# Performance work log

Measured on AMD Instinct MI355X. Metric: run time of the kernel, lower is better.

The kernel has to match this reference:

```python
import jax, jax.numpy as jnp
import numpy as np

B, N, C = 16, 1024, 256

def setup_inputs() -> dict:
    key = jax.random.key(0)
    kq, kk, kv, km, kd = jax.random.split(key, 5)
    query = jax.random.normal(kq, (B, N, C), dtype=jnp.float32)
    key_t = jax.random.normal(kk, (B, N, C), dtype=jnp.float32)
    value = jax.random.normal(kv, (B, N, C), dtype=jnp.float32)
    mask = jax.random.randint(km, (B, N, N), 0, 2).astype(jnp.bool_)
    dis = jax.random.normal(kd, (B, N, N), dtype=jnp.float32)
    return {"query": query, "key": key_t, "value": value, "mask": mask, "dis": dis}

def reference(query, key, value, mask, dis):
    # scores = Q K^T + dis, then scale, mask, softmax, @ V
    scores = jnp.einsum('bqc,bkc->bqk', query, key)
    scores = (scores + dis) / jnp.sqrt(jnp.asarray(query.shape[-1], query.dtype))
    scores = jnp.where(mask, -jnp.inf, scores)
    p_attn = jax.nn.softmax(scores, axis=-1)
    p_val = jnp.einsum('bqk,bkc->bqc', p_attn, value)
    return (p_val, p_attn)
```

## Files before the change

### kernel.cpp

```cpp
#include <hip/hip_runtime.h>
#include <stdint.h>

#define B_ 16
#define N_ 1024
#define C_ 256

typedef __attribute__((ext_vector_type(8))) short short8;
typedef __attribute__((ext_vector_type(4))) float f32x4;

__device__ __forceinline__ short f2bf(float f) {
  uint32_t u = __builtin_bit_cast(uint32_t, f);
  u += 0x7fffu + ((u >> 16) & 1u);
  return (short)(u >> 16);
}

__global__ __launch_bounds__(256) void cast_kernel(const float* __restrict__ in,
                                                   short* __restrict__ out, int n8) {
  int i = blockIdx.x * 256 + threadIdx.x;
  if (i >= n8) return;
  const float4* p = (const float4*)(in + (size_t)i * 8);
  float4 a = p[0], b = p[1];
  short8 r;
  r[0] = f2bf(a.x); r[1] = f2bf(a.y); r[2] = f2bf(a.z); r[3] = f2bf(a.w);
  r[4] = f2bf(b.x); r[5] = f2bf(b.y); r[6] = f2bf(b.z); r[7] = f2bf(b.w);
  *(short8*)(out + (size_t)i * 8) = r;
}

__global__ __launch_bounds__(256) void vt_kernel(const float* __restrict__ V,
                                                 short* __restrict__ Vt) {
  __shared__ float tile[32][33];
  int b = blockIdx.z;
  int nb = blockIdx.x * 32;
  int cb = blockIdx.y * 32;
  int tx = threadIdx.x & 31;
  int ty = threadIdx.x >> 5;
#pragma unroll
  for (int i = 0; i < 32; i += 8)
    tile[ty + i][tx] = V[((size_t)b * N_ + nb + ty + i) * C_ + cb + tx];
  __syncthreads();
#pragma unroll
  for (int i = 0; i < 32; i += 8)
    Vt[((size_t)b * C_ + cb + ty + i) * N_ + nb + tx] = f2bf(tile[tx][ty + i]);
}

__global__ __launch_bounds__(256, 2) void attn_kernel(
    const short* __restrict__ Qbf, const short* __restrict__ Kbf,
    const short* __restrict__ Vt, const float* __restrict__ dis,
    const int* __restrict__ mask, float* __restrict__ p_attn,
    float* __restrict__ p_val) {
  __shared__ short P_lds[16 * 1032];
  __shared__ float red[4][4][4];

  int gid = blockIdx.x;
  int b = (gid & 7) * 2 + ((gid >> 3) & 1);
  int q0 = (gid >> 4) * 16;
  int tid = threadIdx.x;
  int w = tid >> 6;
  int lane = tid & 63;
  int l15 = lane & 15;
  int quad = lane >> 4;

  f32x4 z = {0.f, 0.f, 0.f, 0.f};
  f32x4 acc[16];
#pragma unroll
  for (int i = 0; i < 16; i++) acc[i] = z;

  const short* Qp = Qbf + ((size_t)b * N_ + q0 + l15) * C_ + quad * 8;
  const short* Kp = Kbf + ((size_t)b * N_ + w * 256 + l15) * C_ + quad * 8;

#pragma unroll
  for (int cs = 0; cs < C_; cs += 32) {
    short8 a = *(const short8*)(Qp + cs);
#pragma unroll
    for (int kt = 0; kt < 16; kt++) {
      short8 bf = *(const short8*)(Kp + (size_t)kt * 16 * C_ + cs);
      acc[kt] = __builtin_amdgcn_mfma_f32_16x16x32_bf16(a, bf, acc[kt], 0, 0, 0);
    }
  }

  size_t rb[4];
#pragma unroll
  for (int r = 0; r < 4; r++)
    rb[r] = ((size_t)b * N_ + q0 + quad * 4 + r) * N_ + w * 256 + l15;

  float s[16][4];
  float mrow[4] = {-1e30f, -1e30f, -1e30f, -1e30f};
#pragma unroll
  for (int kc = 0; kc < 4; kc++) {
    float dv[4][4];
    int mv[4][4];
#pragma unroll
    for (int k4 = 0; k4 < 4; k4++)
#pragma unroll
      for (int r = 0; r < 4; r++) {
        size_t idx = rb[r] + (size_t)(kc * 4 + k4) * 16;
        dv[k4][r] = dis[idx];
        mv[k4][r] = mask[idx];
      }
#pragma unroll
    for (int k4 = 0; k4 < 4; k4++)
#pragma unroll
      for (int r = 0; r < 4; r++) {
        int kt = kc * 4 + k4;
        float v = mv[k4][r] ? -3.0e38f : (acc[kt][r] + dv[k4][r]) * 0.0625f;
        s[kt][r] = v;
        mrow[r] = fmaxf(mrow[r], v);
      }
  }

#pragma unroll
  for (int r = 0; r < 4; r++) {
    float m = mrow[r];
    m = fmaxf(m, __shfl_xor(m, 1));
    m = fmaxf(m, __shfl_xor(m, 2));
    m = fmaxf(m, __shfl_xor(m, 4));
    m = fmaxf(m, __shfl_xor(m, 8));
    mrow[r] = m;
  }
  if (l15 == 0) {
#pragma unroll
    for (int r = 0; r < 4; r++) red[w][quad][r] = mrow[r];
  }
  __syncthreads();
  float M[4];
#pragma unroll
  for (int r = 0; r < 4; r++)
    M[r] = fmaxf(fmaxf(red[0][quad][r], red[1][quad][r]),
                 fmaxf(red[2][quad][r], red[3][quad][r]));
  __syncthreads();

  float lsum[4] = {0.f, 0.f, 0.f, 0.f};
#pragma unroll
  for (int kt = 0; kt < 16; kt++)
#pragma unroll
    for (int r = 0; r < 4; r++) {
      float e = __expf(s[kt][r] - M[r]);
      s[kt][r] = e;
      lsum[r] += e;
    }
#pragma unroll
  for (int r = 0; r < 4; r++) {
    float t = lsum[r];
    t += __shfl_xor(t, 1);
    t += __shfl_xor(t, 2);
    t += __shfl_xor(t, 4);
    t += __shfl_xor(t, 8);
    lsum[r] = t;
  }
  if (l15 == 0) {
#pragma unroll
    for (int r = 0; r < 4; r++) red[w][quad][r] = lsum[r];
  }
  __syncthreads();
  float inv[4];
#pragma unroll
  for (int r = 0; r < 4; r++) {
    float L = (red[0][quad][r] + red[1][quad][r]) +
              (red[2][quad][r] + red[3][quad][r]);
    inv[r] = 1.0f / L;
  }

#pragma unroll
  for (int kt = 0; kt < 16; kt++)
#pragma unroll
    for (int r = 0; r < 4; r++) {
      float p = s[kt][r] * inv[r];
      p_attn[rb[r] + (size_t)kt * 16] = p;
      P_lds[(quad * 4 + r) * 1032 + w * 256 + kt * 16 + l15] = f2bf(p);
    }
  __syncthreads();

  f32x4 o[4];
#pragma unroll
  for (int i = 0; i < 4; i++) o[i] = z;
  const short* Vp = Vt + ((size_t)b * C_ + w * 64 + l15) * N_ + quad * 8;

#pragma unroll 4
  for (int ks = 0; ks < N_; ks += 32) {
    short8 a = *(const short8*)&P_lds[l15 * 1032 + ks + quad * 8];
#pragma unroll
    for (int ct = 0; ct < 4; ct++) {
      short8 bf = *(const short8*)(Vp + (size_t)ct * 16 * N_ + ks);
      o[ct] = __builtin_amdgcn_mfma_f32_16x16x32_bf16(a, bf, o[ct], 0, 0, 0);
    }
  }

#pragma unroll
  for (int ct = 0; ct < 4; ct++)
#pragma unroll
    for (int r = 0; r < 4; r++)
      p_val[((size_t)b * N_ + q0 + quad * 4 + r) * C_ + w * 64 + ct * 16 + l15] =
          o[ct][r];
}

extern "C" void kernel_launch(void* const* d_in, const int* in_sizes, int n_in,
                              void* d_out, int out_size, void* d_ws, size_t ws_size,
                              hipStream_t stream) {
  const float* Q   = (const float*)d_in[0];
  const float* K   = (const float*)d_in[1];
  const float* V   = (const float*)d_in[2];
  const int* mask  = (const int*)d_in[3];
  const float* dis = (const float*)d_in[4];

  float* out = (float*)d_out;
  float* p_val  = out;
  float* p_attn = out + (size_t)B_ * N_ * C_;

  const size_t nelem = (size_t)B_ * N_ * C_;
  short* Qbf = (short*)d_ws;
  short* Kbf = Qbf + nelem;
  short* Vt  = Kbf + nelem;

  int n8 = (int)(nelem / 8);
  cast_kernel<<<dim3(n8 / 256), 256, 0, stream>>>(Q, Qbf, n8);
  cast_kernel<<<dim3(n8 / 256), 256, 0, stream>>>(K, Kbf, n8);
  vt_kernel<<<dim3(N_ / 32, C_ / 32, B_), 256, 0, stream>>>(V, Vt);
  attn_kernel<<<dim3(B_ * (N_ / 16)), 256, 0, stream>>>(Qbf, Kbf, Vt, dis, mask,
                                                        p_attn, p_val);
}
```

Before: 335.1 us.

## Transpose score MFMA operands for vectorized dis/mask loads and p_attn stores

Swaps the MFMA operand order in the QK^T step so each lane holds four consecutive key columns for a single query row. This turns the dis/mask loads and the p_attn stores into float4/int4 vector accesses and reduces the row reductions to two cross-quad shuffles plus LDS. It also merges the Q and K casts into one launch, widens the V transpose tiles to 64 with vector loads and stores, raises the launch-bounds occupancy hint to 4, and changes the block-to-batch mapping. The higher occupancy target may force register spilling given the 64-float accumulator array per lane.

```diff
diff --git a/kernel.cpp b/kernel.cpp
--- a/kernel.cpp
+++ b/kernel.cpp
@@ -4,6 +4,7 @@
 #define B_ 16
 #define N_ 1024
 #define C_ 256
+#define LST 1032
 
 typedef __attribute__((ext_vector_type(8))) short short8;
 typedef __attribute__((ext_vector_type(4))) float f32x4;
@@ -14,45 +15,60 @@
   return (short)(u >> 16);
 }
 
-__global__ __launch_bounds__(256) void cast_kernel(const float* __restrict__ in,
-                                                   short* __restrict__ out, int n8) {
-  int i = blockIdx.x * 256 + threadIdx.x;
-  if (i >= n8) return;
-  const float4* p = (const float4*)(in + (size_t)i * 8);
+__global__ __launch_bounds__(256) void cast2_kernel(const float* __restrict__ Q,
+                                                    const float* __restrict__ K,
+                                                    short* __restrict__ Qbf,
+                                                    short* __restrict__ Kbf) {
+  const float* in = blockIdx.y ? K : Q;
+  short* out = blockIdx.y ? Kbf : Qbf;
+  size_t i = (size_t)blockIdx.x * 256 + threadIdx.x;
+  const float4* p = (const float4*)(in + i * 8);
   float4 a = p[0], b = p[1];
   short8 r;
   r[0] = f2bf(a.x); r[1] = f2bf(a.y); r[2] = f2bf(a.z); r[3] = f2bf(a.w);
   r[4] = f2bf(b.x); r[5] = f2bf(b.y); r[6] = f2bf(b.z); r[7] = f2bf(b.w);
-  *(short8*)(out + (size_t)i * 8) = r;
+  *(short8*)(out + i * 8) = r;
 }
 
 __global__ __launch_bounds__(256) void vt_kernel(const float* __restrict__ V,
                                                  short* __restrict__ Vt) {
-  __shared__ float tile[32][33];
+  __shared__ short t[64][72];
   int b = blockIdx.z;
-  int nb = blockIdx.x * 32;
-  int cb = blockIdx.y * 32;
-  int tx = threadIdx.x & 31;
-  int ty = threadIdx.x >> 5;
-#pragma unroll
-  for (int i = 0; i < 32; i += 8)
-    tile[ty + i][tx] = V[((size_t)b * N_ + nb + ty + i) * C_ + cb + tx];
-  __syncthreads();
-#pragma unroll
-  for (int i = 0; i < 32; i += 8)
-    Vt[((size_t)b * C_ + cb + ty + i) * N_ + nb + tx] = f2bf(tile[tx][ty + i]);
-}
-
-__global__ __launch_bounds__(256, 2) void attn_kernel(
+  int nb = blockIdx.x * 64;
+  int cb = blockIdx.y * 64;
+  int tx = threadIdx.x & 15;
+  int ty = threadIdx.x >> 4;
+#pragma unroll
+  for (int i = 0; i < 4; i++) {
+    int n = ty + 16 * i;
+    float4 v = *(const float4*)&V[((size_t)b * N_ + nb + n) * C_ + cb + tx * 4];
+    t[tx * 4 + 0][n] = f2bf(v.x);
+    t[tx * 4 + 1][n] = f2bf(v.y);
+    t[tx * 4 + 2][n] = f2bf(v.z);
+    t[tx * 4 + 3][n] = f2bf(v.w);
+  }
+  __syncthreads();
+  int n0 = (threadIdx.x & 7) * 8;
+  int c0 = threadIdx.x >> 3;
+#pragma unroll
+  for (int i = 0; i < 2; i++) {
+    int c = c0 + 32 * i;
+    short8 s = *(const short8*)&t[c][n0];
+    *(short8*)&Vt[((size_t)b * C_ + cb + c) * N_ + nb + n0] = s;
+  }
+}
+
+__global__ __launch_bounds__(256, 4) void attn_kernel(
     const short* __restrict__ Qbf, const short* __restrict__ Kbf,
     const short* __restrict__ Vt, const float* __restrict__ dis,
     const int* __restrict__ mask, float* __restrict__ p_attn,
     float* __restrict__ p_val) {
-  __shared__ short P_lds[16 * 1032];
-  __shared__ float red[4][4][4];
+  __shared__ short P_lds[16 * LST];
+  __shared__ float redm[4][16];
+  __shared__ float reds[4][16];
 
   int gid = blockIdx.x;
-  int b = (gid & 7) * 2 + ((gid >> 3) & 1);
+  int b = gid & 15;
   int q0 = (gid >> 4) * 16;
   int tid = threadIdx.x;
   int w = tid >> 6;
@@ -70,104 +86,74 @@
 
 #pragma unroll
   for (int cs = 0; cs < C_; cs += 32) {
-    short8 a = *(const short8*)(Qp + cs);
+    short8 bq = *(const short8*)(Qp + cs);
 #pragma unroll
     for (int kt = 0; kt < 16; kt++) {
-      short8 bf = *(const short8*)(Kp + (size_t)kt * 16 * C_ + cs);
-      acc[kt] = __builtin_amdgcn_mfma_f32_16x16x32_bf16(a, bf, acc[kt], 0, 0, 0);
-    }
-  }
-
-  size_t rb[4];
-#pragma unroll
-  for (int r = 0; r < 4; r++)
-    rb[r] = ((size_t)b * N_ + q0 + quad * 4 + r) * N_ + w * 256 + l15;
-
-  float s[16][4];
-  float mrow[4] = {-1e30f, -1e30f, -1e30f, -1e30f};
+      short8 ak = *(const short8*)(Kp + (size_t)kt * 16 * C_ + cs);
+      acc[kt] = __builtin_amdgcn_mfma_f32_16x16x32_bf16(ak, bq, acc[kt], 0, 0, 0);
+    }
+  }
+
+  size_t base = ((size_t)b * N_ + q0 + l15) * N_ + w * 256 + quad * 4;
+
+  float m = -3.0e38f;
 #pragma unroll
   for (int kc = 0; kc < 4; kc++) {
-    float dv[4][4];
-    int mv[4][4];
-#pragma unroll
-    for (int k4 = 0; k4 < 4; k4++)
-#pragma unroll
-      for (int r = 0; r < 4; r++) {
-        size_t idx = rb[r] + (size_t)(kc * 4 + k4) * 16;
-        dv[k4][r] = dis[idx];
-        mv[k4][r] = mask[idx];
-      }
-#pragma unroll
-    for (int k4 = 0; k4 < 4; k4++)
-#pragma unroll
-      for (int r = 0; r < 4; r++) {
-        int kt = kc * 4 + k4;
-        float v = mv[k4][r] ? -3.0e38f : (acc[kt][r] + dv[k4][r]) * 0.0625f;
-        s[kt][r] = v;
-        mrow[r] = fmaxf(mrow[r], v);
-      }
-  }
-
-#pragma unroll
-  for (int r = 0; r < 4; r++) {
-    float m = mrow[r];
-    m = fmaxf(m, __shfl_xor(m, 1));
-    m = fmaxf(m, __shfl_xor(m, 2));
-    m = fmaxf(m, __shfl_xor(m, 4));
-    m = fmaxf(m, __shfl_xor(m, 8));
-    mrow[r] = m;
-  }
-  if (l15 == 0) {
-#pragma unroll
-    for (int r = 0; r < 4; r++) red[w][quad][r] = mrow[r];
-  }
-  __syncthreads();
-  float M[4];
-#pragma unroll
-  for (int r = 0; r < 4; r++)
-    M[r] = fmaxf(fmaxf(red[0][quad][r], red[1][quad][r]),
-                 fmaxf(red[2][quad][r], red[3][quad][r]));
-  __syncthreads();
-
-  float lsum[4] = {0.f, 0.f, 0.f, 0.f};
-#pragma unroll
-  for (int kt = 0; kt < 16; kt++)
+    float4 dv[4];
+    int4 mv[4];
+#pragma unroll
+    for (int j = 0; j < 4; j++)
+      dv[j] = *(const float4*)(dis + base + (size_t)(kc * 4 + j) * 16);
+#pragma unroll
+    for (int j = 0; j < 4; j++)
+      mv[j] = *(const int4*)(mask + base + (size_t)(kc * 4 + j) * 16);
+#pragma unroll
+    for (int j = 0; j < 4; j++) {
+      int kt = kc * 4 + j;
+      acc[kt][0] = mv[j].x ? -3.0e38f : (acc[kt][0] + dv[j].x) * 0.0625f;
+      acc[kt][1] = mv[j].y ? -3.0e38f : (acc[kt][1] + dv[j].y) * 0.0625f;
+      acc[kt][2] = mv[j].z ? -3.0e38f : (acc[kt][2] + dv[j].z) * 0.0625f;
+      acc[kt][3] = mv[j].w ? -3.0e38f : (acc[kt][3] + dv[j].w) * 0.0625f;
+      m = fmaxf(m, fmaxf(fmaxf(acc[kt][0], acc[kt][1]),
+                         fmaxf(acc[kt][2], acc[kt][3])));
+    }
+  }
+
+  m = fmaxf(m, __shfl_xor(m, 16));
+  m = fmaxf(m, __shfl_xor(m, 32));
+  if (lane < 16) redm[w][lane] = m;
+  __syncthreads();
+  float M = fmaxf(fmaxf(redm[0][l15], redm[1][l15]),
+                  fmaxf(redm[2][l15], redm[3][l15]));
+
+  float sum = 0.f;
+#pragma unroll
+  for (int kt = 0; kt < 16; kt++) {
 #pragma unroll
     for (int r = 0; r < 4; r++) {
-      float e = __expf(s[kt][r] - M[r]);
-      s[kt][r] = e;
-      lsum[r] += e;
-    }
-#pragma unroll
-  for (int r = 0; r < 4; r++) {
-    float t = lsum[r];
-    t += __shfl_xor(t, 1);
-    t += __shfl_xor(t, 2);
-    t += __shfl_xor(t, 4);
-    t += __shfl_xor(t, 8);
-    lsum[r] = t;
-  }
-  if (l15 == 0) {
-#pragma unroll
-    for (int r = 0; r < 4; r++) red[w][quad][r] = lsum[r];
-  }
-  __syncthreads();
-  float inv[4];
-#pragma unroll
-  for (int r = 0; r < 4; r++) {
-    float L = (red[0][quad][r] + red[1][quad][r]) +
-              (red[2][quad][r] + red[3][quad][r]);
-    inv[r] = 1.0f / L;
-  }
-
-#pragma unroll
-  for (int kt = 0; kt < 16; kt++)
-#pragma unroll
-    for (int r = 0; r < 4; r++) {
-      float p = s[kt][r] * inv[r];
-      p_attn[rb[r] + (size_t)kt * 16] = p;
-      P_lds[(quad * 4 + r) * 1032 + w * 256 + kt * 16 + l15] = f2bf(p);
-    }
+      float e = __expf(acc[kt][r] - M);
+      acc[kt][r] = e;
+      sum += e;
+    }
+  }
+  sum += __shfl_xor(sum, 16);
+  sum += __shfl_xor(sum, 32);
+  if (lane < 16) reds[w][lane] = sum;
+  __syncthreads();
+  float inv = 1.0f / (reds[0][l15] + reds[1][l15] + reds[2][l15] + reds[3][l15]);
+
+#pragma unroll
+  for (int kt = 0; kt < 16; kt++) {
+    float4 p;
+    p.x = acc[kt][0] * inv;
+    p.y = acc[kt][1] * inv;
+    p.z = acc[kt][2] * inv;
+    p.w = acc[kt][3] * inv;
+    *(float4*)(p_attn + base + (size_t)kt * 16) = p;
+    short4 pb;
+    pb.x = f2bf(p.x); pb.y = f2bf(p.y); pb.z = f2bf(p.z); pb.w = f2bf(p.w);
+    *(short4*)&P_lds[l15 * LST + w * 256 + kt * 16 + quad * 4] = pb;
+  }
   __syncthreads();
 
   f32x4 o[4];
@@ -177,11 +163,11 @@
 
 #pragma unroll 4
   for (int ks = 0; ks < N_; ks += 32) {
-    short8 a = *(const short8*)&P_lds[l15 * 1032 + ks + quad * 8];
+    short8 a = *(const short8*)&P_lds[l15 * LST + ks + quad * 8];
 #pragma unroll
     for (int ct = 0; ct < 4; ct++) {
-      short8 bf = *(const short8*)(Vp + (size_t)ct * 16 * N_ + ks);
-      o[ct] = __builtin_amdgcn_mfma_f32_16x16x32_bf16(a, bf, o[ct], 0, 0, 0);
+      short8 bv = *(const short8*)(Vp + (size_t)ct * 16 * N_ + ks);
+      o[ct] = __builtin_amdgcn_mfma_f32_16x16x32_bf16(a, bv, o[ct], 0, 0, 0);
     }
   }
 
@@ -211,10 +197,8 @@
   short* Kbf = Qbf + nelem;
   short* Vt  = Kbf + nelem;
 
-  int n8 = (int)(nelem / 8);
-  cast_kernel<<<dim3(n8 / 256), 256, 0, stream>>>(Q, Qbf, n8);
-  cast_kernel<<<dim3(n8 / 256), 256, 0, stream>>>(K, Kbf, n8);
-  vt_kernel<<<dim3(N_ / 32, C_ / 32, B_), 256, 0, stream>>>(V, Vt);
+  cast2_kernel<<<dim3((unsigned)(nelem / 8 / 256), 2), 256, 0, stream>>>(Q, K, Qbf, Kbf);
+  vt_kernel<<<dim3(N_ / 64, C_ / 64, B_), 256, 0, stream>>>(V, Vt);
   attn_kernel<<<dim3(B_ * (N_ / 16)), 256, 0, stream>>>(Qbf, Kbf, Vt, dis, mask,
                                                         p_attn, p_val);
 }
```

New measurement: 375.5 us. 12.1% more time.
